# Kernel optimization log

Hardware: AMD Instinct MI355X
Metric: run time of the kernel (lower is better)

## Reference

```python
import jax, jax.numpy as jnp
import numpy as np

B, T, E = 4, 2048, 2048
NH, NKV, HD = 16, 4, 128
THETA = 10000.0


def _rope(x, pos_ids, theta):
    # x: [b, h, t, hd]; pos_ids: [b, t]; theta: [hd/2]
    ang = pos_ids[:, None, :, None].astype(jnp.float32) * theta  # [b,1,t,hd/2]
    cos, sin = jnp.cos(ang), jnp.sin(ang)
    x1, x2 = x[..., ::2], x[..., 1::2]
    # interleave rotated pairs back to [..., hd]
    rot = jnp.stack([x1 * cos - x2 * sin, x1 * sin + x2 * cos], axis=-1)
    return rot.reshape(x.shape)


def setup_inputs() -> dict:
    key = jax.random.key(0)
    ks = jax.random.split(key, 10)
    s = 0.02
    x = jax.random.normal(ks[0], (B, T, E), dtype=jnp.float32)
    attention_mask = jax.random.randint(ks[1], (B, T, T), 0, 2, dtype=jnp.int32)
    # torch nn.Linear weights stored here as [in, out] (y = x @ W + b)
    Wq = jax.random.normal(ks[2], (E, E), dtype=jnp.float32) * s
    bq = jnp.zeros((E,), dtype=jnp.float32)
    Wk = jax.random.normal(ks[3], (E, NKV * HD), dtype=jnp.float32) * s
    bk = jnp.zeros((NKV * HD,), dtype=jnp.float32)
    Wv = jax.random.normal(ks[4], (E, NKV * HD), dtype=jnp.float32) * s
    bv = jnp.zeros((NKV * HD,), dtype=jnp.float32)
    Wo = jax.random.normal(ks[5], (E, E), dtype=jnp.float32) * s
    bo = jnp.zeros((E,), dtype=jnp.float32)
    return {"x": x, "attention_mask": attention_mask, "Wq": Wq, "bq": bq,
            "Wk": Wk, "bk": bk, "Wv": Wv, "bv": bv, "Wo": Wo, "bo": bo}


def reference(x, attention_mask, Wq, bq, Wk, bk, Wv, bv, Wo, bo):
    b, t = x.shape[0], x.shape[1]
    # faithful to original: plain reshape (view), NOT transpose-based head split
    q = (x @ Wq + bq).reshape(b, NH, t, HD)
    k = (x @ Wk + bk).reshape(b, NKV, t, HD)
    v = (x @ Wv + bv).reshape(b, NKV, t, HD)
    theta = THETA ** (-jnp.arange(0, HD, 2, dtype=jnp.float32) / HD)
    pos = jnp.broadcast_to(jnp.arange(t), (b, t))
    # original RoPE.forward is wrapped in @torch.no_grad() -> stop_gradient
    k = jax.lax.stop_gradient(_rope(k, pos, theta))
    v = jax.lax.stop_gradient(_rope(v, pos, theta))  # note: RoPE applied to V too
    g = NH // NKV
    k = jnp.tile(k, (1, g, 1, 1))  # torch .repeat tiles kv heads
    v = jnp.tile(v, (1, g, 1, 1))
    # original divides by head_dim ** (-0.5) == multiply by sqrt(head_dim)
    scores = jnp.einsum('bhqd,bhkd->bhqk', q, k) * (HD ** 0.5)
    scores = jnp.where(attention_mask[:, None, :, :] == 0, jnp.float32(1e-9), scores)
    attn = jax.nn.softmax(scores, axis=-1)  # dropout inactive (eval mode)
    out = jnp.einsum('bhqk,bhkd->bhqd', attn, v)
    out = out.transpose(0, 2, 1, 3).reshape(b, t, NH * HD)
    return out @ Wo + bo
```

## Files before the change

kernel.cpp:

```cpp
#include <hip/hip_runtime.h>
#include <math.h>

constexpr int Bc   = 4;
constexpr int Tc   = 2048;
constexpr int Ec   = 2048;
constexpr int NHc  = 16;
constexpr int NKVc = 4;
constexpr int HDc  = 128;
constexpr int KVEc = NKVc * HDc;

typedef __attribute__((ext_vector_type(8))) short bf16x8;
typedef __attribute__((ext_vector_type(4))) short short4v;
typedef __attribute__((ext_vector_type(4))) float f32x4;

__device__ __forceinline__ short f2bf(float f) {
    union { float f; unsigned u; } v; v.f = f;
    unsigned r = v.u + 0x7FFF + ((v.u >> 16) & 1);
    return (short)(r >> 16);
}
__device__ __forceinline__ float bf2f(short s) {
    union { unsigned u; float f; } v; v.u = ((unsigned)(unsigned short)s) << 16;
    return v.f;
}
__device__ __forceinline__ float ex2(float x) {
    float r; asm("v_exp_f32 %0, %1" : "=v"(r) : "v"(x)); return r;
}
__device__ __forceinline__ void gload16(const void* g, void* l) {
    __builtin_amdgcn_global_load_lds(
        (const __attribute__((address_space(1))) unsigned*)g,
        (__attribute__((address_space(3))) unsigned*)l, 16, 0, 0);
}

__global__ __launch_bounds__(256)
void convert_split(const float* __restrict__ X, short* __restrict__ Xhi,
                   short* __restrict__ Xlo)
{
    int i = blockIdx.x * 256 + threadIdx.x;
    float4 v = ((const float4*)X)[i];
    float fv[4] = {v.x, v.y, v.z, v.w};
    short4v hi, lo;
    #pragma unroll
    for (int j = 0; j < 4; ++j) {
        hi[j] = f2bf(fv[j]);
        lo[j] = f2bf(fv[j] - bf2f(hi[j]));
    }
    ((short4v*)Xhi)[i] = hi;
    ((short4v*)Xlo)[i] = lo;
}

__global__ __launch_bounds__(256)
void transpose_split(const float* __restrict__ W, short* __restrict__ WThi,
                     short* __restrict__ WTlo, int K, int N)
{
    __shared__ float Ls[32][33];
    const int k0 = blockIdx.x * 32, n0 = blockIdx.y * 32;
    const int t = threadIdx.x;
    const int r = t >> 3, c4 = (t & 7) << 2;
    float4 v = *(const float4*)(W + (size_t)(k0 + r) * N + n0 + c4);
    Ls[r][c4 + 0] = v.x; Ls[r][c4 + 1] = v.y;
    Ls[r][c4 + 2] = v.z; Ls[r][c4 + 3] = v.w;
    __syncthreads();
    short4v hi, lo;
    #pragma unroll
    for (int i = 0; i < 4; ++i) {
        float f = Ls[c4 + i][r];
        hi[i] = f2bf(f);
        lo[i] = f2bf(f - bf2f(hi[i]));
    }
    *(short4v*)(WThi + (size_t)(n0 + r) * K + k0 + c4) = hi;
    if (WTlo) *(short4v*)(WTlo + (size_t)(n0 + r) * K + k0 + c4) = lo;
}

__global__ __launch_bounds__(256)
void mask_bits(const int* __restrict__ mask, unsigned long long* __restrict__ Mb)
{
    const int widx = blockIdx.x * 4 + (threadIdx.x >> 6);
    const int L = threadIdx.x & 63;
    const int m = mask[(size_t)widx * 64 + L];
    unsigned long long bits = __ballot(m != 0);
    if (L == 0) Mb[widx] = bits;
}

template <bool SPLIT>
__global__ __launch_bounds__(256, 2)
void gemm_mfma(const short* __restrict__ Ahi, const short* __restrict__ Alo,
               const short* __restrict__ Bhi, const short* __restrict__ Blo,
               const float* __restrict__ bias, float* __restrict__ C,
               int M, int N, int K)
{
    __shared__ short AsH[128 * 32];
    __shared__ short BsH[128 * 32];
    __shared__ short AsL[SPLIT ? 128 * 32 : 8];
    __shared__ short BsL[SPLIT ? 128 * 32 : 8];

    const int t = threadIdx.x;
    const int w = t >> 6, L = t & 63;
    const int l16 = L & 15, quad = L >> 4;
    const int wr = w >> 1, wc = w & 1;
    const int bm = blockIdx.x * 128, bn = blockIdx.y * 128;

    const int sm = L >> 2;
    const int sq = ((L & 3) - (sm >> 2)) & 3;
    const int scol = sq * 8;

    f32x4 acc[4][4];
    #pragma unroll
    for (int mi = 0; mi < 4; ++mi)
        #pragma unroll
        for (int ni = 0; ni < 4; ++ni) acc[mi][ni] = (f32x4){0, 0, 0, 0};

    const int fxor = (quad + (l16 >> 2)) & 3;

    for (int k0 = 0; k0 < K; k0 += 32) {
        __syncthreads();
        #pragma unroll
        for (int i = 0; i < 2; ++i) {
            const int wl = w * 2 + i;
            const size_t ra = (size_t)(bm + wl * 16 + sm) * K + k0 + scol;
            const size_t rb = (size_t)(bn + wl * 16 + sm) * K + k0 + scol;
            gload16(Ahi + ra, &AsH[wl * 512]);
            gload16(Bhi + rb, &BsH[wl * 512]);
            if (SPLIT) {
                gload16(Alo + ra, &AsL[wl * 512]);
                gload16(Blo + rb, &BsL[wl * 512]);
            }
        }
        __syncthreads();

        bf16x8 ah[4], bh[4], al[4], bl[4];
        #pragma unroll
        for (int mi = 0; mi < 4; ++mi) {
            const int ch = ((wr * 4 + mi) * 64 + l16 * 4 + fxor) * 8;
            ah[mi] = *(const bf16x8*)&AsH[ch];
            if (SPLIT) al[mi] = *(const bf16x8*)&AsL[ch];
        }
        #pragma unroll
        for (int ni = 0; ni < 4; ++ni) {
            const int ch = ((wc * 4 + ni) * 64 + l16 * 4 + fxor) * 8;
            bh[ni] = *(const bf16x8*)&BsH[ch];
            if (SPLIT) bl[ni] = *(const bf16x8*)&BsL[ch];
        }
        #pragma unroll
        for (int mi = 0; mi < 4; ++mi)
            #pragma unroll
            for (int ni = 0; ni < 4; ++ni) {
                acc[mi][ni] = __builtin_amdgcn_mfma_f32_16x16x32_bf16(
                    ah[mi], bh[ni], acc[mi][ni], 0, 0, 0);
                if (SPLIT) {
                    acc[mi][ni] = __builtin_amdgcn_mfma_f32_16x16x32_bf16(
                        al[mi], bh[ni], acc[mi][ni], 0, 0, 0);
                    acc[mi][ni] = __builtin_amdgcn_mfma_f32_16x16x32_bf16(
                        ah[mi], bl[ni], acc[mi][ni], 0, 0, 0);
                }
            }
    }

    #pragma unroll
    for (int ni = 0; ni < 4; ++ni) {
        const int col = bn + wc * 64 + ni * 16 + l16;
        const float bv = bias[col];
        #pragma unroll
        for (int mi = 0; mi < 4; ++mi) {
            #pragma unroll
            for (int r = 0; r < 4; ++r) {
                const int row = bm + wr * 64 + mi * 16 + quad * 4 + r;
                C[(size_t)row * N + col] = acc[mi][ni][r] + bv;
            }
        }
    }
}

__global__ __launch_bounds__(256)
void rope_k(const float* __restrict__ X2d, short* __restrict__ Khi,
            short* __restrict__ Klo)
{
    const int idx = blockIdx.x * 256 + threadIdx.x;
    const int j  = idx & 63;
    const int tk = (idx >> 6) & (Tc - 1);
    const int kh = (idx >> 17) & (NKVc - 1);
    const int bb = idx >> 19;
    const int row = (kh << 9) + (tk >> 2);
    const int col = ((tk & 3) << 7) + (j << 1);
    const float* src = X2d + ((size_t)bb * Tc + row) * KVEc + col;
    const float a = src[0];
    const float b = src[1];
    const float theta = powf(10000.0f, -(float)j * (1.0f / 64.0f));
    const float ang = (float)tk * theta;
    float s, c;
    sincosf(ang, &s, &c);
    const float r0 = a * c - b * s;
    const float r1 = a * s + b * c;
    const size_t off = (((size_t)bb * NKVc + kh) * Tc + tk) * HDc + (j << 1);
    short h0 = f2bf(r0), h1 = f2bf(r1);
    Khi[off]     = h0;  Klo[off]     = f2bf(r0 - bf2f(h0));
    Khi[off + 1] = h1;  Klo[off + 1] = f2bf(r1 - bf2f(h1));
}

__global__ __launch_bounds__(256)
void rope_v_t(const float* __restrict__ V2d, short* __restrict__ Vt)
{
    __shared__ short Ls[128][40];
    const int g  = blockIdx.x;
    const int kh = blockIdx.y;
    const int bb = blockIdx.z;
    const int t  = threadIdx.x;

    const float* src = V2d + ((size_t)bb * Tc + (kh << 9) + (g << 3)) * KVEc;
    #pragma unroll
    for (int i = 0; i < 4; ++i) {
        int e = i * 256 + t;
        float4 v = ((const float4*)src)[e];
        int row = e >> 7;
        int col = (e & 127) << 2;
        int tkl = (row << 2) + (col >> 7);
        int d0  = col & 127;
        int tk  = (g << 5) + tkl;
        float fv[4] = {v.x, v.y, v.z, v.w};
        #pragma unroll
        for (int p = 0; p < 2; ++p) {
            int j = (d0 >> 1) + p;
            float theta = powf(10000.0f, -(float)j * (1.0f / 64.0f));
            float ang = (float)tk * theta;
            float s, c;
            sincosf(ang, &s, &c);
            float a = fv[2 * p], b = fv[2 * p + 1];
            Ls[d0 + 2 * p    ][tkl] = f2bf(a * c - b * s);
            Ls[d0 + 2 * p + 1][tkl] = f2bf(a * s + b * c);
        }
    }
    __syncthreads();
    const int d = t >> 1;
    const int h16 = (t & 1) << 4;
    short* dst = Vt + (((size_t)bb * NKVc + kh) * HDc + d) * Tc + (g << 5) + h16;
    bf16x8 o0 = *(const bf16x8*)&Ls[d][h16];
    bf16x8 o1 = *(const bf16x8*)&Ls[d][h16 + 8];
    *(bf16x8*)dst = o0;
    *(bf16x8*)(dst + 8) = o1;
}

#define SM_AND_P(S, MR, LPV, OACC, MW, AK0, AK1)                               \
  do {                                                                         \
    const unsigned mlo_ = (unsigned)(MW);                                      \
    const unsigned mhi_ = (unsigned)((MW) >> 32);                              \
    const int gq_ = quad << 2;                                                 \
    const unsigned fm_0 = mlo_ >> gq_, fm_1 = (mlo_ >> 16) >> gq_;             \
    const unsigned fm_2 = mhi_ >> gq_, fm_3 = (mhi_ >> 16) >> gq_;             \
    _Pragma("unroll")                                                          \
    for (int r_ = 0; r_ < 4; ++r_) {                                           \
      S[0][r_] = (fm_0 & (1u << r_)) ? S[0][r_] * SCALE2 : MASKED2;            \
      S[1][r_] = (fm_1 & (1u << r_)) ? S[1][r_] * SCALE2 : MASKED2;            \
      S[2][r_] = (fm_2 & (1u << r_)) ? S[2][r_] * SCALE2 : MASKED2;            \
      S[3][r_] = (fm_3 & (1u << r_)) ? S[3][r_] * SCALE2 : MASKED2;            \
    }                                                                          \
    float mt_;                                                                 \
    {                                                                          \
      float a0_ = fmaxf(fmaxf(S[0][0], S[0][1]), fmaxf(S[0][2], S[0][3]));     \
      float a1_ = fmaxf(fmaxf(S[1][0], S[1][1]), fmaxf(S[1][2], S[1][3]));     \
      float a2_ = fmaxf(fmaxf(S[2][0], S[2][1]), fmaxf(S[2][2], S[2][3]));     \
      float a3_ = fmaxf(fmaxf(S[3][0], S[3][1]), fmaxf(S[3][2], S[3][3]));     \
      mt_ = fmaxf(fmaxf(a0_, a1_), fmaxf(a2_, a3_));                           \
    }                                                                          \
    mt_ = fmaxf(mt_, __shfl_xor(mt_, 16));                                     \
    mt_ = fmaxf(mt_, __shfl_xor(mt_, 32));                                     \
    const bool res_ = (mt_ > (MR) + 8.0f);                                     \
    if (__any(res_)) {                                                         \
      const float mn_ = res_ ? mt_ : (MR);                                     \
      const float alq_ = ex2((MR) - mn_);                                      \
      MR = mn_;                                                                \
      LPV *= alq_;                                                             \
      float alo_0 = __shfl(alq_, quad * 20 + 0);                               \
      float alo_1 = __shfl(alq_, quad * 20 + 1);                               \
      float alo_2 = __shfl(alq_, quad * 20 + 2);                               \
      float alo_3 = __shfl(alq_, quad * 20 + 3);                               \
      _Pragma("unroll")                                                        \
      for (int nc_ = 0; nc_ < 8; ++nc_) {                                      \
        OACC[nc_][0] *= alo_0; OACC[nc_][1] *= alo_1;                          \
        OACC[nc_][2] *= alo_2; OACC[nc_][3] *= alo_3;                          \
      }                                                                        \
    }                                                                          \
    {                                                                          \
      float t0_ = 0.f, t1_ = 0.f;                                              \
      _Pragma("unroll")                                                        \
      for (int nt_ = 0; nt_ < 4; ++nt_) {                                      \
        float p0_ = ex2(S[nt_][0] - (MR));                                     \
        float p1_ = ex2(S[nt_][1] - (MR));                                     \
        float p2_ = ex2(S[nt_][2] - (MR));                                     \
        float p3_ = ex2(S[nt_][3] - (MR));                                     \
        S[nt_][0] = p0_; S[nt_][1] = p1_;                                      \
        S[nt_][2] = p2_; S[nt_][3] = p3_;                                      \
        t0_ += p0_ + p1_; t1_ += p2_ + p3_;                                    \
      }                                                                        \
      LPV += t0_ + t1_;                                                        \
    }                                                                          \
    int pk00_, pk01_, pk10_, pk11_, pk20_, pk21_, pk30_, pk31_;                \
    asm("v_cvt_pk_bf16_f32 %0, %1, %2" : "=v"(pk00_) : "v"(S[0][0]), "v"(S[0][1])); \
    asm("v_cvt_pk_bf16_f32 %0, %1, %2" : "=v"(pk01_) : "v"(S[0][2]), "v"(S[0][3])); \
    asm("v_cvt_pk_bf16_f32 %0, %1, %2" : "=v"(pk10_) : "v"(S[1][0]), "v"(S[1][1])); \
    asm("v_cvt_pk_bf16_f32 %0, %1, %2" : "=v"(pk11_) : "v"(S[1][2]), "v"(S[1][3])); \
    asm("v_cvt_pk_bf16_f32 %0, %1, %2" : "=v"(pk20_) : "v"(S[2][0]), "v"(S[2][1])); \
    asm("v_cvt_pk_bf16_f32 %0, %1, %2" : "=v"(pk21_) : "v"(S[2][2]), "v"(S[2][3])); \
    asm("v_cvt_pk_bf16_f32 %0, %1, %2" : "=v"(pk30_) : "v"(S[3][0]), "v"(S[3][1])); \
    asm("v_cvt_pk_bf16_f32 %0, %1, %2" : "=v"(pk31_) : "v"(S[3][2]), "v"(S[3][3])); \
    {                                                                          \
      int u0_, u1_;                                                            \
      u0_ = __shfl(pk00_, srcA); u1_ = __shfl(pk10_, srcA); AK0.d[0] = q1v ? u1_ : u0_; \
      u0_ = __shfl(pk01_, srcA); u1_ = __shfl(pk11_, srcA); AK0.d[1] = q1v ? u1_ : u0_; \
      u0_ = __shfl(pk00_, srcB); u1_ = __shfl(pk10_, srcB); AK0.d[2] = q1v ? u1_ : u0_; \
      u0_ = __shfl(pk01_, srcB); u1_ = __shfl(pk11_, srcB); AK0.d[3] = q1v ? u1_ : u0_; \
      u0_ = __shfl(pk20_, srcA); u1_ = __shfl(pk30_, srcA); AK1.d[0] = q1v ? u1_ : u0_; \
      u0_ = __shfl(pk21_, srcA); u1_ = __shfl(pk31_, srcA); AK1.d[1] = q1v ? u1_ : u0_; \
      u0_ = __shfl(pk20_, srcB); u1_ = __shfl(pk30_, srcB); AK1.d[2] = q1v ? u1_ : u0_; \
      u0_ = __shfl(pk21_, srcB); u1_ = __shfl(pk31_, srcB); AK1.d[3] = q1v ? u1_ : u0_; \
    }                                                                          \
  } while (0)

__global__ __launch_bounds__(256, 2)
void attn_mfma(const float* __restrict__ Q2d, const short* __restrict__ Khi_g,
               const short* __restrict__ Klo_g, const short* __restrict__ Vt_g,
               const unsigned long long* __restrict__ Mb, short* __restrict__ AObf)
{
    __shared__ short KhiS[64 * 128];
    __shared__ short KloS[64 * 128];
    __shared__ short VtS [128 * 64];

    const int fid  = blockIdx.x + 16 * (blockIdx.y + 16 * blockIdx.z);
    const int slot = fid >> 3;
    const int grp  = (fid & 7) + 8 * (slot >> 4);
    const int qb   = slot & 15;
    const int h    = grp & 15;
    const int bb   = grp >> 4;

    const int t    = threadIdx.x;
    const int w    = t >> 6;
    const int L    = t & 63;
    const int l16  = L & 15;
    const int quad = L >> 4;
    const int q1v  = quad >> 1;
    const int kh   = h & (NKVc - 1);
    const int tq0  = qb * 128 + w * 16;
    const int tq1  = tq0 + 64;

    bf16x8 qhi0[4], qlo0[4], qhi1[4], qlo1[4];
    {
        const float* qbase = Q2d +
            ((size_t)(bb * Tc + h * HDc + qb * 8 + w)) * Ec + 128 * l16;
        #pragma unroll
        for (int kc = 0; kc < 4; ++kc) {
            const float* p0 = qbase + kc * 32 + quad * 8;
            const float* p1 = p0 + (size_t)4 * Ec;
            #pragma unroll
            for (int j = 0; j < 8; ++j) {
                float f0 = p0[j];
                short h0 = f2bf(f0);
                qhi0[kc][j] = h0;
                qlo0[kc][j] = f2bf(f0 - bf2f(h0));
                float f1 = p1[j];
                short h1 = f2bf(f1);
                qhi1[kc][j] = h1;
                qlo1[kc][j] = f2bf(f1 - bf2f(h1));
            }
        }
    }

    float m0 = -INFINITY, lp0 = 0.0f;
    float m1 = -INFINITY, lp1 = 0.0f;
    f32x4 o0[8], o1[8];
    #pragma unroll
    for (int nc = 0; nc < 8; ++nc) {
        o0[nc] = (f32x4){0, 0, 0, 0};
        o1[nc] = (f32x4){0, 0, 0, 0};
    }

    const short* kbh = Khi_g + ((size_t)(bb * NKVc + kh)) * Tc * HDc;
    const short* kbl = Klo_g + ((size_t)(bb * NKVc + kh)) * Tc * HDc;
    const short* vb  = Vt_g  + ((size_t)(bb * NKVc + kh)) * HDc * Tc;
    const unsigned long long* mrow0 =
        Mb + ((size_t)(bb * Tc + tq0 + l16)) * (Tc / 64);
    const unsigned long long* mrow1 = mrow0 + (size_t)64 * (Tc / 64);

    constexpr float SCALE2  = 11.313708498984761f * 1.4426950408889634f;
    constexpr float MASKED2 = 1e-9f * 1.4426950408889634f;

    const int km   = L >> 4;
    const int kpos = L & 15;
    const int vm   = L >> 3;
    const int vc   = ((L & 7) - vm) & 7;

    const int srcA = l16 + 16 * ((2 * quad)     & 3);
    const int srcB = l16 + 16 * ((2 * quad + 1) & 3);

    auto stageK = [&](int kt) {
        #pragma unroll
        for (int i = 0; i < 4; ++i) {
            const int wl = w * 4 + i;
            const int krow = wl * 4 + km;
            const int kc_ = (kpos - (krow & 15)) & 15;
            const size_t go = (size_t)(kt * 64 + krow) * HDc + kc_ * 8;
            gload16(kbh + go, &KhiS[wl * 512]);
            gload16(kbl + go, &KloS[wl * 512]);
        }
    };
    auto stageV = [&](int kt) {
        #pragma unroll
        for (int i = 0; i < 4; ++i) {
            const int wl = w * 4 + i;
            const int vrow = wl * 8 + vm;
            gload16(vb + (size_t)vrow * Tc + kt * 64 + vc * 8, &VtS[wl * 512]);
        }
    };

    asm volatile("s_waitcnt vmcnt(0)" ::: "memory");
    __builtin_amdgcn_sched_barrier(0);
    stageK(0);
    __builtin_amdgcn_sched_barrier(0);
    stageV(0);
    __builtin_amdgcn_sched_barrier(0);
    unsigned long long mw0 = mrow0[0];
    unsigned long long mw1 = mrow1[0];
    __builtin_amdgcn_sched_barrier(0);

    union U { int d[4]; bf16x8 v; };

    for (int kt = 0; kt < Tc / 64; ++kt) {
        const int ktn = (kt + 1) & 31;

        asm volatile("s_waitcnt vmcnt(6)" ::: "memory");
        __builtin_amdgcn_s_barrier();
        __builtin_amdgcn_sched_barrier(0);

        f32x4 s0[4], s1[4];
        #pragma unroll
        for (int nt = 0; nt < 4; ++nt) {
            f32x4 a0 = (f32x4){0, 0, 0, 0};
            f32x4 a1 = (f32x4){0, 0, 0, 0};
            #pragma unroll
            for (int kc = 0; kc < 4; ++kc) {
                const int ch = (((nt * 4 + (l16 >> 2)) << 6) + ((l16 & 3) << 4)
                                + ((kc * 4 + quad + l16) & 15)) << 3;
                bf16x8 khiF = *(const bf16x8*)&KhiS[ch];
                bf16x8 kloF = *(const bf16x8*)&KloS[ch];
                a0 = __builtin_amdgcn_mfma_f32_16x16x32_bf16(khiF, qhi0[kc], a0, 0, 0, 0);
                a0 = __builtin_amdgcn_mfma_f32_16x16x32_bf16(khiF, qlo0[kc], a0, 0, 0, 0);
                a0 = __builtin_amdgcn_mfma_f32_16x16x32_bf16(kloF, qhi0[kc], a0, 0, 0, 0);
                a1 = __builtin_amdgcn_mfma_f32_16x16x32_bf16(khiF, qhi1[kc], a1, 0, 0, 0);
                a1 = __builtin_amdgcn_mfma_f32_16x16x32_bf16(khiF, qlo1[kc], a1, 0, 0, 0);
                a1 = __builtin_amdgcn_mfma_f32_16x16x32_bf16(kloF, qhi1[kc], a1, 0, 0, 0);
            }
            s0[nt] = a0;
            s1[nt] = a1;
        }

        asm volatile("s_waitcnt lgkmcnt(0)" ::: "memory");
        __builtin_amdgcn_sched_barrier(0);
        __builtin_amdgcn_s_barrier();
        __builtin_amdgcn_sched_barrier(0);
        stageK(ktn);
        __builtin_amdgcn_sched_barrier(0);

        U A00, A01, A10, A11;
        SM_AND_P(s0, m0, lp0, o0, mw0, A00, A01);
        SM_AND_P(s1, m1, lp1, o1, mw1, A10, A11);

        asm volatile("s_waitcnt vmcnt(8)" ::: "memory");
        __builtin_amdgcn_s_barrier();
        __builtin_amdgcn_sched_barrier(0);

        #pragma unroll
        for (int nc = 0; nc < 8; ++nc) {
            const int rg = (nc * 2 + (l16 >> 3)) << 6;
            const int rm = l16 & 7;
            const int ch0 = (rg + (rm << 3) + ((quad + rm) & 7)) << 3;
            const int ch1 = (rg + (rm << 3) + ((quad + 4 + rm) & 7)) << 3;
            bf16x8 b0 = *(const bf16x8*)&VtS[ch0];
            bf16x8 b1 = *(const bf16x8*)&VtS[ch1];
            o0[nc] = __builtin_amdgcn_mfma_f32_16x16x32_bf16(A00.v, b0, o0[nc], 0, 0, 0);
            o0[nc] = __builtin_amdgcn_mfma_f32_16x16x32_bf16(A01.v, b1, o0[nc], 0, 0, 0);
            o1[nc] = __builtin_amdgcn_mfma_f32_16x16x32_bf16(A10.v, b0, o1[nc], 0, 0, 0);
            o1[nc] = __builtin_amdgcn_mfma_f32_16x16x32_bf16(A11.v, b1, o1[nc], 0, 0, 0);
        }

        asm volatile("s_waitcnt lgkmcnt(0)" ::: "memory");
        __builtin_amdgcn_sched_barrier(0);
        __builtin_amdgcn_s_barrier();
        __builtin_amdgcn_sched_barrier(0);
        stageV(ktn);
        __builtin_amdgcn_sched_barrier(0);
        mw0 = mrow0[ktn];
        mw1 = mrow1[ktn];
        __builtin_amdgcn_sched_barrier(0);
    }

    asm volatile("s_waitcnt vmcnt(0)" ::: "memory");

    lp0 += __shfl_xor(lp0, 16);
    lp0 += __shfl_xor(lp0, 32);
    lp1 += __shfl_xor(lp1, 16);
    lp1 += __shfl_xor(lp1, 32);
    const float invl0 = 1.0f / lp0;
    const float invl1 = 1.0f / lp1;
    float invo0[4], invo1[4];
    #pragma unroll
    for (int r = 0; r < 4; ++r) {
        invo0[r] = __shfl(invl0, quad * 16 + quad * 4 + r);
        invo1[r] = __shfl(invl1, quad * 16 + quad * 4 + r);
    }

    #pragma unroll
    for (int r = 0; r < 4; ++r) {
        short* orow = AObf + ((size_t)(bb * Tc + tq0 + quad * 4 + r)) * Ec
                           + h * HDc + l16;
        #pragma unroll
        for (int nc = 0; nc < 8; ++nc)
            orow[nc * 16] = f2bf(o0[nc][r] * invo0[r]);
    }
    #pragma unroll
    for (int r = 0; r < 4; ++r) {
        short* orow = AObf + ((size_t)(bb * Tc + tq1 + quad * 4 + r)) * Ec
                           + h * HDc + l16;
        #pragma unroll
        for (int nc = 0; nc < 8; ++nc)
            orow[nc * 16] = f2bf(o1[nc][r] * invo1[r]);
    }
}

extern "C" void kernel_launch(void* const* d_in, const int* in_sizes, int n_in,
                              void* d_out, int out_size, void* d_ws, size_t ws_size,
                              hipStream_t stream)
{
    const float* x    = (const float*)d_in[0];
    const int*  amask = (const int*)  d_in[1];
    const float* Wq   = (const float*)d_in[2];
    const float* bq   = (const float*)d_in[3];
    const float* Wk   = (const float*)d_in[4];
    const float* bk   = (const float*)d_in[5];
    const float* Wv   = (const float*)d_in[6];
    const float* bv   = (const float*)d_in[7];
    const float* Wo   = (const float*)d_in[8];
    const float* bo   = (const float*)d_in[9];
    float* out = (float*)d_out;

    char* ws = (char*)d_ws;
    float* Q2d   = (float*)(ws);
    short* Xhi   = (short*)(ws + 67108864);
    short* Xlo   = (short*)(ws + 100663296);
    short* WqThi = (short*)(ws + 134217728);
    short* WqTlo = (short*)(ws + 134217728 + 8388608);
    float* K2d   = (float*)(ws + 150994944);
    float* V2d   = (float*)(ws + 100663296);
    short* Khi   = (short*)(ws + 100663296 + 16777216);
    short* Klo   = (short*)(ws + 100663296 + 25165824);
    short* WkThi = (short*)(ws + 134217728);
    short* WkTlo = (short*)(ws + 134217728 + 2097152);
    short* WvThi = (short*)(ws + 134217728 + 4194304);
    short* WoThi = (short*)(ws + 134217728 + 8388608);
    short* Vt    = (short*)(ws + 150994944);
    short* AObf  = (short*)(ws + 67108864);
    unsigned long long* Mb = (unsigned long long*)(ws + 167772160);

    const int M = Bc * Tc;
    dim3 blk(256);

    mask_bits<<<(Bc * Tc * (Tc / 64)) / 4, blk, 0, stream>>>(amask, Mb);
    transpose_split<<<dim3(Ec / 32, Ec / 32), blk, 0, stream>>>(Wq, WqThi, WqTlo, Ec, Ec);
    convert_split<<<(M * Ec / 4) / 256, blk, 0, stream>>>(x, Xhi, Xlo);
    gemm_mfma<true><<<dim3(M / 128, Ec / 128), blk, 0, stream>>>(
        Xhi, Xlo, WqThi, WqTlo, bq, Q2d, M, Ec, Ec);
    transpose_split<<<dim3(Ec / 32, KVEc / 32), blk, 0, stream>>>(Wk, WkThi, WkTlo, Ec, KVEc);
    transpose_split<<<dim3(Ec / 32, KVEc / 32), blk, 0, stream>>>(Wv, WvThi, nullptr, Ec, KVEc);
    transpose_split<<<dim3(Ec / 32, Ec / 32), blk, 0, stream>>>(Wo, WoThi, nullptr, Ec, Ec);
    gemm_mfma<true><<<dim3(M / 128, KVEc / 128), blk, 0, stream>>>(
        Xhi, Xlo, WkThi, WkTlo, bk, K2d, M, KVEc, Ec);
    gemm_mfma<false><<<dim3(M / 128, KVEc / 128), blk, 0, stream>>>(
        Xhi, nullptr, WvThi, nullptr, bv, V2d, M, KVEc, Ec);
    rope_k<<<(Bc * NKVc * Tc * 64) / 256, blk, 0, stream>>>(K2d, Khi, Klo);
    rope_v_t<<<dim3(Tc / 32, NKVc, Bc), blk, 0, stream>>>(V2d, Vt);
    attn_mfma<<<dim3(Tc / 128, NHc, Bc), blk, 0, stream>>>(
        Q2d, Khi, Klo, Vt, Mb, AObf);
    gemm_mfma<false><<<dim3(M / 128, Ec / 128), blk, 0, stream>>>(
        AObf, nullptr, WoThi, nullptr, bo, out, M, Ec, Ec);
}
```

Measured before the change: 1.082 ms.

## Emit Q as bf16 hi/lo from projection GEMM and restructure attention loads

The Q projection GEMM now writes its result directly as bf16 hi/lo pairs, so attention loads pre-split Q with 16-byte vector loads instead of reading fp32 and splitting per element. Attention launch bounds are raised to 3 blocks per SM. The mask-word loads move to the top of each iteration and the vmcnt waits are rearranged. Risks include register spills from the tighter launch bound, the GEMM epilogue issuing two scattered short stores per element, and the vmcnt accounting no longer matching the outstanding loads.

```diff
diff --git a/kernel.cpp b/kernel.cpp
--- a/kernel.cpp
+++ b/kernel.cpp
@@ -81,11 +81,12 @@
     if (L == 0) Mb[widx] = bits;
 }
 
-template <bool SPLIT>
+template <bool SPLIT, bool QOUT>
 __global__ __launch_bounds__(256, 2)
 void gemm_mfma(const short* __restrict__ Ahi, const short* __restrict__ Alo,
                const short* __restrict__ Bhi, const short* __restrict__ Blo,
                const float* __restrict__ bias, float* __restrict__ C,
+               short* __restrict__ Chi, short* __restrict__ Clo,
                int M, int N, int K)
 {
     __shared__ short AsH[128 * 32];
@@ -164,7 +165,14 @@
             #pragma unroll
             for (int r = 0; r < 4; ++r) {
                 const int row = bm + wr * 64 + mi * 16 + quad * 4 + r;
-                C[(size_t)row * N + col] = acc[mi][ni][r] + bv;
+                const float f = acc[mi][ni][r] + bv;
+                if (QOUT) {
+                    const short hi = f2bf(f);
+                    Chi[(size_t)row * N + col] = hi;
+                    Clo[(size_t)row * N + col] = f2bf(f - bf2f(hi));
+                } else {
+                    C[(size_t)row * N + col] = f;
+                }
             }
         }
     }
@@ -314,9 +322,10 @@
     }                                                                          \
   } while (0)
 
-__global__ __launch_bounds__(256, 2)
-void attn_mfma(const float* __restrict__ Q2d, const short* __restrict__ Khi_g,
-               const short* __restrict__ Klo_g, const short* __restrict__ Vt_g,
+__global__ __launch_bounds__(256, 3)
+void attn_mfma(const short* __restrict__ Qhi_g, const short* __restrict__ Qlo_g,
+               const short* __restrict__ Khi_g, const short* __restrict__ Klo_g,
+               const short* __restrict__ Vt_g,
                const unsigned long long* __restrict__ Mb, short* __restrict__ AObf)
 {
     __shared__ short KhiS[64 * 128];
@@ -342,23 +351,16 @@
 
     bf16x8 qhi0[4], qlo0[4], qhi1[4], qlo1[4];
     {
-        const float* qbase = Q2d +
-            ((size_t)(bb * Tc + h * HDc + qb * 8 + w)) * Ec + 128 * l16;
+        const size_t qoff = (size_t)(bb * Tc + h * HDc + qb * 8 + w) * Ec
+                          + 128 * l16 + quad * 8;
+        const short* qh = Qhi_g + qoff;
+        const short* ql = Qlo_g + qoff;
         #pragma unroll
         for (int kc = 0; kc < 4; ++kc) {
-            const float* p0 = qbase + kc * 32 + quad * 8;
-            const float* p1 = p0 + (size_t)4 * Ec;
-            #pragma unroll
-            for (int j = 0; j < 8; ++j) {
-                float f0 = p0[j];
-                short h0 = f2bf(f0);
-                qhi0[kc][j] = h0;
-                qlo0[kc][j] = f2bf(f0 - bf2f(h0));
-                float f1 = p1[j];
-                short h1 = f2bf(f1);
-                qhi1[kc][j] = h1;
-                qlo1[kc][j] = f2bf(f1 - bf2f(h1));
-            }
+            qhi0[kc] = *(const bf16x8*)(qh + kc * 32);
+            qlo0[kc] = *(const bf16x8*)(ql + kc * 32);
+            qhi1[kc] = *(const bf16x8*)(qh + (size_t)4 * Ec + kc * 32);
+            qlo1[kc] = *(const bf16x8*)(ql + (size_t)4 * Ec + kc * 32);
         }
     }
 
@@ -415,18 +417,18 @@
     __builtin_amdgcn_sched_barrier(0);
     stageV(0);
     __builtin_amdgcn_sched_barrier(0);
-    unsigned long long mw0 = mrow0[0];
-    unsigned long long mw1 = mrow1[0];
-    __builtin_amdgcn_sched_barrier(0);
 
     union U { int d[4]; bf16x8 v; };
 
     for (int kt = 0; kt < Tc / 64; ++kt) {
         const int ktn = (kt + 1) & 31;
 
-        asm volatile("s_waitcnt vmcnt(6)" ::: "memory");
+        asm volatile("s_waitcnt vmcnt(4)" ::: "memory");
         __builtin_amdgcn_s_barrier();
         __builtin_amdgcn_sched_barrier(0);
+
+        const unsigned long long mw0 = mrow0[kt];
+        const unsigned long long mw1 = mrow1[kt];
 
         f32x4 s0[4], s1[4];
         #pragma unroll
@@ -457,11 +459,12 @@
         stageK(ktn);
         __builtin_amdgcn_sched_barrier(0);
 
+        asm volatile("s_waitcnt vmcnt(8)" ::: "memory");
+
         U A00, A01, A10, A11;
         SM_AND_P(s0, m0, lp0, o0, mw0, A00, A01);
         SM_AND_P(s1, m1, lp1, o1, mw1, A10, A11);
 
-        asm volatile("s_waitcnt vmcnt(8)" ::: "memory");
         __builtin_amdgcn_s_barrier();
         __builtin_amdgcn_sched_barrier(0);
 
@@ -485,9 +488,6 @@
         __builtin_amdgcn_sched_barrier(0);
         stageV(ktn);
         __builtin_amdgcn_sched_barrier(0);
-        mw0 = mrow0[ktn];
-        mw1 = mrow1[ktn];
-        __builtin_amdgcn_sched_barrier(0);
     }
 
     asm volatile("s_waitcnt vmcnt(0)" ::: "memory");
@@ -540,7 +540,8 @@
     float* out = (float*)d_out;
 
     char* ws = (char*)d_ws;
-    float* Q2d   = (float*)(ws);
+    short* Qhi   = (short*)(ws);
+    short* Qlo   = (short*)(ws + 33554432);
     short* Xhi   = (short*)(ws + 67108864);
     short* Xlo   = (short*)(ws + 100663296);
     short* WqThi = (short*)(ws + 134217728);
@@ -563,19 +564,19 @@
     mask_bits<<<(Bc * Tc * (Tc / 64)) / 4, blk, 0, stream>>>(amask, Mb);
     transpose_split<<<dim3(Ec / 32, Ec / 32), blk, 0, stream>>>(Wq, WqThi, WqTlo, Ec, Ec);
     convert_split<<<(M * Ec / 4) / 256, blk, 0, stream>>>(x, Xhi, Xlo);
-    gemm_mfma<true><<<dim3(M / 128, Ec / 128), blk, 0, stream>>>(
-        Xhi, Xlo, WqThi, WqTlo, bq, Q2d, M, Ec, Ec);
+    gemm_mfma<true, true><<<dim3(M / 128, Ec / 128), blk, 0, stream>>>(
+        Xhi, Xlo, WqThi, WqTlo, bq, nullptr, Qhi, Qlo, M, Ec, Ec);
     transpose_split<<<dim3(Ec / 32, KVEc / 32), blk, 0, stream>>>(Wk, WkThi, WkTlo, Ec, KVEc);
     transpose_split<<<dim3(Ec / 32, KVEc / 32), blk, 0, stream>>>(Wv, WvThi, nullptr, Ec, KVEc);
     transpose_split<<<dim3(Ec / 32, Ec / 32), blk, 0, stream>>>(Wo, WoThi, nullptr, Ec, Ec);
-    gemm_mfma<true><<<dim3(M / 128, KVEc / 128), blk, 0, stream>>>(
-        Xhi, Xlo, WkThi, WkTlo, bk, K2d, M, KVEc, Ec);
-    gemm_mfma<false><<<dim3(M / 128, KVEc / 128), blk, 0, stream>>>(
-        Xhi, nullptr, WvThi, nullptr, bv, V2d, M, KVEc, Ec);
+    gemm_mfma<true, false><<<dim3(M / 128, KVEc / 128), blk, 0, stream>>>(
+        Xhi, Xlo, WkThi, WkTlo, bk, K2d, nullptr, nullptr, M, KVEc, Ec);
+    gemm_mfma<false, false><<<dim3(M / 128, KVEc / 128), blk, 0, stream>>>(
+        Xhi, nullptr, WvThi, nullptr, bv, V2d, nullptr, nullptr, M, KVEc, Ec);
     rope_k<<<(Bc * NKVc * Tc * 64) / 256, blk, 0, stream>>>(K2d, Khi, Klo);
     rope_v_t<<<dim3(Tc / 32, NKVc, Bc), blk, 0, stream>>>(V2d, Vt);
     attn_mfma<<<dim3(Tc / 128, NHc, Bc), blk, 0, stream>>>(
-        Q2d, Khi, Klo, Vt, Mb, AObf);
-    gemm_mfma<false><<<dim3(M / 128, Ec / 128), blk, 0, stream>>>(
-        AObf, nullptr, WoThi, nullptr, bo, out, M, Ec, Ec);
-}
+        Qhi, Qlo, Khi, Klo, Vt, Mb, AObf);
+    gemm_mfma<false, false><<<dim3(M / 128, Ec / 128), blk, 0, stream>>>(
+        AObf, nullptr, WoThi, nullptr, bo, out, nullptr, nullptr, M, Ec, Ec);
+}
```

Result: slower. 1.969 ms (+82.0%).
